# Kernel tuning notes

Measured on AMD Instinct MI355X. Metric: run time of the kernel, lower is better.

Reference implementation:

```python
import jax, jax.numpy as jnp
import numpy as np

T, B, D, H = 256, 64, 1024, 1024


def setup_inputs() -> dict:
    key = jax.random.key(0)
    ks = jax.random.split(key, 12)
    stdv = 1.0 / np.sqrt(H)
    u = lambda k, shape: jax.random.uniform(k, shape, jnp.float32, -stdv, stdv)
    return {
        "input_": jax.random.normal(ks[0], (T, B, D), jnp.float32),
        "length": jax.random.randint(ks[1], (B,), 1, T + 1, jnp.int32),
        "h0": jnp.zeros((B, H), jnp.float32),
        "cj": jax.random.normal(ks[2], (B, H), jnp.float32),
        "he": jax.random.normal(ks[3], (B, H), jnp.float32),
        "w_ih": u(ks[4], (3 * H, D)),
        "w_hh": u(ks[5], (3 * H, H)),
        "w_ch": u(ks[6], (3 * H, H)),
        "w_zh": u(ks[7], (3 * H, H)),
        "b_ih": u(ks[8], (3 * H,)),
        "b_hh": u(ks[9], (3 * H,)),
        "b_ch": u(ks[10], (3 * H,)),
        "b_zh": u(ks[11], (3 * H,)),
    }


def _chunk3(g):
    # mirrors torch .chunk(3, 1) on a (..., 3H) tensor
    return g[..., :H], g[..., H:2 * H], g[..., 2 * H:]


def reference(input_, length, h0, cj, he, w_ih, w_hh, w_ch, w_zh,
              b_ih, b_hh, b_ch, b_zh):
    # context projections are time-invariant: hoist out of the recurrence
    c_r, c_i, c_n = _chunk3(cj @ w_ch.T + b_ch)   # (B,H) each
    z_r, z_i, z_n = _chunk3(he @ w_zh.T + b_zh)   # (B,H) each
    # input projections for all steps at once: (T,B,3H)
    gi_all = jnp.einsum('tbd,gd->tbg', input_, w_ih) + b_ih

    def step(h, xs):
        gi_t, t = xs
        i_r, i_i, i_n = _chunk3(gi_t)
        h_r, h_i, h_n_ = _chunk3(h @ w_hh.T + b_hh)
        resetgate = jax.nn.sigmoid(i_r + h_r + c_r + z_r)
        inputgate = jax.nn.sigmoid(i_i + h_i + c_i + z_i)
        newgate = jnp.tanh(i_n + resetgate * h_n_ + c_n + z_n)
        hy = newgate + inputgate * (h - newgate)
        mask = (t < length).astype(hy.dtype)[:, None]          # (B,1)
        # NOTE: faithful to original torch code, which uses hx[0]
        # (first batch row, broadcast) in the masked branch.
        h_next = hy * mask + h[0] * (1.0 - mask)
        return h_next, h_next

    h_last, output = jax.lax.scan(step, h0, (gi_all, jnp.arange(T)))
    h_n = h_last[None]  # (num_layers=1, B, H)
    return output, h_n
```

## Files before the change

### kernel.cpp

```cpp
#include <hip/hip_runtime.h>
#include <stdint.h>

#define TT 256
#define BB 64
#define DD 1024
#define HH 1024
#define G3 3072

typedef unsigned long long ull;
typedef __attribute__((ext_vector_type(8))) short short8;
typedef __attribute__((ext_vector_type(4))) float f32x4;

__device__ __forceinline__ unsigned short f2bf(float f) {
  union { float f; unsigned int i; } v; v.f = f;
  unsigned int x = v.i;
  return (unsigned short)((x + 0x7fffu + ((x >> 16) & 1u)) >> 16);
}
__device__ __forceinline__ float bf2f(unsigned short u) {
  union { unsigned int i; float f; } v; v.i = ((unsigned int)u) << 16; return v.f;
}
__device__ __forceinline__ f32x4 mfma16(short8 a, short8 b, f32x4 c) {
  return __builtin_amdgcn_mfma_f32_16x16x32_bf16(a, b, c, 0, 0, 0);
}
__device__ __forceinline__ void gload_lds16(const void* g, void* l) {
  __builtin_amdgcn_global_load_lds((const __attribute__((address_space(1))) void*)g,
                                   (__attribute__((address_space(3))) void*)l,
                                   16, 0, 0);
}
__device__ __forceinline__ short8 mall_load16(const unsigned short* p) {
  short8 r;
  asm volatile("global_load_dwordx4 %0, %1, off sc0 sc1" : "=v"(r) : "v"(p));
  return r;
}

__global__ void k_cvt_bf16(const float* __restrict__ in, unsigned short* __restrict__ out, int n4) {
  int i = blockIdx.x * blockDim.x + threadIdx.x;
  int stride = gridDim.x * blockDim.x;
  for (; i < n4; i += stride) {
    float4 v = ((const float4*)in)[i];
    ushort4 o;
    o.x = f2bf(v.x); o.y = f2bf(v.y); o.z = f2bf(v.z); o.w = f2bf(v.w);
    ((ushort4*)out)[i] = o;
  }
}

__global__ __launch_bounds__(256) void k_ctx(
    const unsigned short* __restrict__ cjb, const unsigned short* __restrict__ heb,
    const unsigned short* __restrict__ Wchb, const unsigned short* __restrict__ Wzhb,
    const float* __restrict__ b_ih, const float* __restrict__ b_hh,
    const float* __restrict__ b_ch, const float* __restrict__ b_zh,
    float* __restrict__ E) {
  __shared__ f32x4 red[4][4][64];
  int n0 = blockIdx.x * 16;
  int tid = threadIdx.x;
  int w = tid >> 6, l = tid & 63, lo = l & 15, hi = l >> 4;
  f32x4 acc[4];
#pragma unroll
  for (int r = 0; r < 4; r++) acc[r] = (f32x4){0.f, 0.f, 0.f, 0.f};
#pragma unroll 4
  for (int kk = 0; kk < 16; kk++) {
    int k = w * 512 + kk * 32;
    const unsigned short* Asrc = (k < 1024) ? cjb : heb;
    const unsigned short* Bsrc = (k < 1024) ? Wchb : Wzhb;
    int kw = (k < 1024) ? k : (k - 1024);
    int kof = kw + hi * 8;
    short8 bf = *(const short8*)(Bsrc + (size_t)(n0 + lo) * 1024 + kof);
#pragma unroll
    for (int r = 0; r < 4; r++) {
      short8 af = *(const short8*)(Asrc + (size_t)(r * 16 + lo) * 1024 + kof);
      acc[r] = mfma16(af, bf, acc[r]);
    }
  }
#pragma unroll
  for (int r = 0; r < 4; r++) red[w][r][l] = acc[r];
  __syncthreads();
  f32x4 s = red[0][w][l];
#pragma unroll
  for (int w2 = 1; w2 < 4; w2++) {
    f32x4 p = red[w2][w][l];
    s[0] += p[0]; s[1] += p[1]; s[2] += p[2]; s[3] += p[3];
  }
  int g = n0 + lo;
  float bias = b_ih[g] + b_ch[g] + b_zh[g] + ((g < 2048) ? b_hh[g] : 0.0f);
#pragma unroll
  for (int j = 0; j < 4; j++) {
    int b = w * 16 + hi * 4 + j;
    E[(size_t)b * G3 + g] = s[j] + bias;
  }
}

__global__ __launch_bounds__(256) void k_gemm_gi(
    const unsigned short* __restrict__ Xb,
    const unsigned short* __restrict__ Wb,
    const float* __restrict__ E,
    unsigned short* __restrict__ gi) {
  __shared__ unsigned short As[128 * 32];
  __shared__ unsigned short Bs[128 * 32];
  int bid = blockIdx.x;
  int mt = bid & 127;
  int nt = bid >> 7;
  int m0 = mt * 128, n0 = nt * 128;
  int tid = threadIdx.x;
  int w = tid >> 6, l = tid & 63, lo = l & 15, hi = l >> 4;
  int wr = w >> 1, wc = w & 1;
  f32x4 acc[4][4];
#pragma unroll
  for (int i = 0; i < 4; i++)
#pragma unroll
    for (int j = 0; j < 4; j++) acc[i][j] = (f32x4){0.f, 0.f, 0.f, 0.f};
  int srow = tid >> 2;
  int scol = (tid & 3) * 8;
  for (int kt = 0; kt < 32; kt++) {
    int k0 = kt * 32;
    __syncthreads();
    gload_lds16(Xb + (size_t)(m0 + srow) * 1024 + k0 + scol, As + srow * 32 + scol);
    gload_lds16(Xb + (size_t)(m0 + 64 + srow) * 1024 + k0 + scol, As + (64 + srow) * 32 + scol);
    gload_lds16(Wb + (size_t)(n0 + srow) * 1024 + k0 + scol, Bs + srow * 32 + scol);
    gload_lds16(Wb + (size_t)(n0 + 64 + srow) * 1024 + k0 + scol, Bs + (64 + srow) * 32 + scol);
    asm volatile("s_waitcnt vmcnt(0)" ::: "memory");
    __syncthreads();
    short8 a[4], b[4];
#pragma unroll
    for (int i = 0; i < 4; i++) a[i] = *(const short8*)(As + (wr * 64 + i * 16 + lo) * 32 + hi * 8);
#pragma unroll
    for (int i = 0; i < 4; i++) b[i] = *(const short8*)(Bs + (wc * 64 + i * 16 + lo) * 32 + hi * 8);
#pragma unroll
    for (int i = 0; i < 4; i++)
#pragma unroll
      for (int j = 0; j < 4; j++) acc[i][j] = mfma16(a[i], b[j], acc[i][j]);
  }
#pragma unroll
  for (int i = 0; i < 4; i++)
#pragma unroll
    for (int j = 0; j < 4; j++)
#pragma unroll
      for (int e = 0; e < 4; e++) {
        int r = m0 + wr * 64 + i * 16 + hi * 4 + e;
        int c = n0 + wc * 64 + j * 16 + lo;
        float v = acc[i][j][e] + E[(size_t)(r & 63) * G3 + c];
        gi[(size_t)r * G3 + c] = f2bf(v);
      }
}

__global__ __launch_bounds__(128) void k_rnn(
    const unsigned short* __restrict__ giE,
    const unsigned short* __restrict__ Whhb,
    const float* __restrict__ b_hh,
    const float* __restrict__ h0,
    const int* __restrict__ length,
    unsigned short* __restrict__ hbuf,
    float* __restrict__ out,
    float* __restrict__ hn,
    unsigned int* __restrict__ seq) {
  extern __shared__ char smem[];
  unsigned short* wlds = (unsigned short*)smem;
  float* h0f = (float*)(smem + 98304);

  const int cs = blockIdx.x, j0 = cs * 16;
  const int tid = threadIdx.x;
  const int w = tid >> 6, l = tid & 63, lo = l & 15, hi = l >> 4;
  const int rowbase = w * 32;
  const int col = j0 + lo;

#pragma unroll
  for (int k2 = 0; k2 < 16; ++k2) {
    int kk = w * 16 + k2;
#pragma unroll
    for (int s = 0; s < 3; ++s) {
      int f = kk * 3 + s;
      short8 v = *(const short8*)(Whhb + (size_t)(s * 1024 + j0 + lo) * 1024 + kk * 32 + hi * 8);
      ((short8*)wlds)[f * 64 + l] = v;
    }
  }
  const float bhhn = b_hh[2048 + col];
  float hA[4], hB[4];
  int lenA[4], lenB[4];
#pragma unroll
  for (int j = 0; j < 4; ++j) {
    int rA = rowbase + hi * 4 + j, rB = rA + 16;
    hA[j] = h0[(size_t)rA * 1024 + col]; lenA[j] = length[rA];
    hB[j] = h0[(size_t)rB * 1024 + col]; lenB[j] = length[rB];
  }
  {
    unsigned short* dst = hbuf + (size_t)cs * 1024;
#pragma unroll
    for (int j = 0; j < 4; ++j) {
      unsigned int mA = f2bf(hA[j]), mB = f2bf(hB[j]);
      unsigned int oA = __shfl_xor(mA, 1, 64), oB = __shfl_xor(mB, 1, 64);
      if (!(lo & 1)) {
        int rr = rowbase + hi * 4 + j;
        __hip_atomic_store((unsigned int*)(dst + rr * 16 + lo), mA | (oA << 16),
                           __ATOMIC_RELAXED, __HIP_MEMORY_SCOPE_AGENT);
        __hip_atomic_store((unsigned int*)(dst + (rr + 16) * 16 + lo), mB | (oB << 16),
                           __ATOMIC_RELAXED, __HIP_MEMORY_SCOPE_AGENT);
      }
    }
  }
  if (w == 0 && hi == 0) h0f[lo] = hA[0];
  __syncthreads();
  asm volatile("s_waitcnt vmcnt(0)" ::: "memory");
  if (l == 0)
    __hip_atomic_store(&seq[(cs * 2 + w) * 16], 1u, __ATOMIC_RELAXED, __HIP_MEMORY_SCOPE_AGENT);
  unsigned short gir[24];
#pragma unroll
  for (int r2 = 0; r2 < 2; ++r2)
#pragma unroll
    for (int s = 0; s < 3; ++s)
#pragma unroll
      for (int j = 0; j < 4; ++j)
        gir[(r2 * 3 + s) * 4 + j] =
            giE[(size_t)(rowbase + r2 * 16 + hi * 4 + j) * G3 + s * 1024 + col];

#define ISSUE(c, X)                                                                    \
  _Pragma("unroll") for (int k2 = 0; k2 < 8; ++k2) {                                   \
    int kk = (c) * 8 + k2;                                                             \
    size_t cb = (size_t)(kk * 2 + (hi >> 1));                                          \
    X[k2 * 2 + 0] = mall_load16(base + (cb * 64 + rowbase + lo) * 16 + (hi & 1) * 8);  \
    X[k2 * 2 + 1] = mall_load16(base + (cb * 64 + rowbase + 16 + lo) * 16 + (hi & 1) * 8); \
  }
#define WAITV(N)                                                                       \
  asm volatile("s_waitcnt vmcnt(" #N ")" ::: "memory");                                \
  __builtin_amdgcn_sched_barrier(0)
#define CRUNCH(c, X)                                                                   \
  _Pragma("unroll") for (int k2 = 0; k2 < 8; ++k2) {                                   \
    int kk = (c) * 8 + k2;                                                             \
    const short8* wf = ((const short8*)wlds) + (size_t)(kk * 3) * 64 + l;              \
    short8 b0 = wf[0], b1 = wf[64], b2 = wf[128];                                      \
    a00 = mfma16(X[k2 * 2 + 0], b0, a00);                                              \
    a01 = mfma16(X[k2 * 2 + 0], b1, a01);                                              \
    a02 = mfma16(X[k2 * 2 + 0], b2, a02);                                              \
    a10 = mfma16(X[k2 * 2 + 1], b0, a10);                                              \
    a11 = mfma16(X[k2 * 2 + 1], b1, a11);                                              \
    a12 = mfma16(X[k2 * 2 + 1], b2, a12);                                              \
  }

  for (int t = 0; t < TT; ++t) {
    {
      const unsigned int* sp0 = seq + (size_t)(2 * l) * 16;
      const unsigned int* sp1 = sp0 + 16;
      unsigned int tgt = (unsigned int)(t + 1);
      for (;;) {
        unsigned int v0 = __hip_atomic_load(sp0, __ATOMIC_RELAXED, __HIP_MEMORY_SCOPE_AGENT);
        unsigned int v1 = __hip_atomic_load(sp1, __ATOMIC_RELAXED, __HIP_MEMORY_SCOPE_AGENT);
        if (__all((v0 >= tgt) && (v1 >= tgt))) break;
        __builtin_amdgcn_s_sleep(1);
      }
    }
    const unsigned short* base = hbuf + ((size_t)(t & 1) * 64) * 1024;
    f32x4 a00 = {0.f, 0.f, 0.f, 0.f}, a01 = a00, a02 = a00, a10 = a00, a11 = a00, a12 = a00;
    {
      short8 XA[16], XB[16];
      ISSUE(0, XA);
      ISSUE(1, XB);
      WAITV(16);
      CRUNCH(0, XA);
      ISSUE(2, XA);
      WAITV(16);
      CRUNCH(1, XB);
      ISSUE(3, XB);
      WAITV(16);
      CRUNCH(2, XA);
      WAITV(0);
      CRUNCH(3, XB);
    }
    float h0p = (w == 0) ? __shfl(hA[0], lo, 64) : h0f[(t & 1) * 16 + lo];
    float rA[4], rB[4];
#pragma unroll
    for (int j = 0; j < 4; ++j) {
      float R = a00[j] + bf2f(gir[0 * 4 + j]);
      float I = a01[j] + bf2f(gir[1 * 4 + j]);
      float rg = 1.f / (1.f + __expf(-R));
      float ig = 1.f / (1.f + __expf(-I));
      float nx = bf2f(gir[2 * 4 + j]) + rg * (a02[j] + bhhn);
      nx = fminf(15.f, fmaxf(-15.f, nx));
      float e2 = __expf(2.f * nx);
      float ng = (e2 - 1.f) / (e2 + 1.f);
      float hy = ng + ig * (hA[j] - ng);
      rA[j] = (t < lenA[j]) ? hy : h0p;
    }
#pragma unroll
    for (int j = 0; j < 4; ++j) {
      float R = a10[j] + bf2f(gir[(3 + 0) * 4 + j]);
      float I = a11[j] + bf2f(gir[(3 + 1) * 4 + j]);
      float rg = 1.f / (1.f + __expf(-R));
      float ig = 1.f / (1.f + __expf(-I));
      float nx = bf2f(gir[(3 + 2) * 4 + j]) + rg * (a12[j] + bhhn);
      nx = fminf(15.f, fmaxf(-15.f, nx));
      float e2 = __expf(2.f * nx);
      float ng = (e2 - 1.f) / (e2 + 1.f);
      float hy = ng + ig * (hB[j] - ng);
      rB[j] = (t < lenB[j]) ? hy : h0p;
    }
#pragma unroll
    for (int j = 0; j < 4; ++j) { hA[j] = rA[j]; hB[j] = rB[j]; }
    if (t < TT - 1) {
      unsigned short* dst = hbuf + ((size_t)((t + 1) & 1) * 64 + cs) * 1024;
#pragma unroll
      for (int j = 0; j < 4; ++j) {
        unsigned int mA = f2bf(hA[j]), mB = f2bf(hB[j]);
        unsigned int oA = __shfl_xor(mA, 1, 64), oB = __shfl_xor(mB, 1, 64);
        if (!(lo & 1)) {
          int rr = rowbase + hi * 4 + j;
          __hip_atomic_store((unsigned int*)(dst + rr * 16 + lo), mA | (oA << 16),
                             __ATOMIC_RELAXED, __HIP_MEMORY_SCOPE_AGENT);
          __hip_atomic_store((unsigned int*)(dst + (rr + 16) * 16 + lo), mB | (oB << 16),
                             __ATOMIC_RELAXED, __HIP_MEMORY_SCOPE_AGENT);
        }
      }
      if (w == 0 && hi == 0) h0f[((t + 1) & 1) * 16 + lo] = hA[0];
      asm volatile("s_waitcnt vmcnt(0) lgkmcnt(0)" ::: "memory");
      if (l == 0)
        __hip_atomic_store(&seq[(cs * 2 + w) * 16], (unsigned int)(t + 2),
                           __ATOMIC_RELAXED, __HIP_MEMORY_SCOPE_AGENT);
#pragma unroll
      for (int j = 0; j < 4; ++j) {
        int rr = rowbase + hi * 4 + j;
        out[(size_t)t * (BB * HH) + (size_t)rr * 1024 + col] = rA[j];
        out[(size_t)t * (BB * HH) + (size_t)(rr + 16) * 1024 + col] = rB[j];
      }
      const unsigned short* gb = giE + (size_t)(t + 1) * 64 * G3;
#pragma unroll
      for (int r2 = 0; r2 < 2; ++r2)
#pragma unroll
        for (int s = 0; s < 3; ++s)
#pragma unroll
          for (int j = 0; j < 4; ++j)
            gir[(r2 * 3 + s) * 4 + j] =
                gb[(size_t)(rowbase + r2 * 16 + hi * 4 + j) * G3 + s * 1024 + col];
    } else {
#pragma unroll
      for (int j = 0; j < 4; ++j) {
        int rr = rowbase + hi * 4 + j;
        out[(size_t)t * (BB * HH) + (size_t)rr * 1024 + col] = rA[j];
        out[(size_t)t * (BB * HH) + (size_t)(rr + 16) * 1024 + col] = rB[j];
        hn[(size_t)rr * 1024 + col] = rA[j];
        hn[(size_t)(rr + 16) * 1024 + col] = rB[j];
      }
    }
  }
#undef ISSUE
#undef WAITV
#undef CRUNCH
}

extern "C" void kernel_launch(void* const* d_in, const int* in_sizes, int n_in,
                              void* d_out, int out_size, void* d_ws, size_t ws_size,
                              hipStream_t stream) {
  const float* input_ = (const float*)d_in[0];
  const int* length   = (const int*)d_in[1];
  const float* h0     = (const float*)d_in[2];
  const float* cj     = (const float*)d_in[3];
  const float* he     = (const float*)d_in[4];
  const float* w_ih   = (const float*)d_in[5];
  const float* w_hh   = (const float*)d_in[6];
  const float* w_ch   = (const float*)d_in[7];
  const float* w_zh   = (const float*)d_in[8];
  const float* b_ih   = (const float*)d_in[9];
  const float* b_hh   = (const float*)d_in[10];
  const float* b_ch   = (const float*)d_in[11];
  const float* b_zh   = (const float*)d_in[12];

  char* ws = (char*)d_ws;
  const size_t OFF_SEQ   = 0;
  const size_t OFF_HBUF  = 16384;
  const size_t OFF_XB    = 524288;
  const size_t OFF_WIHB  = OFF_XB + 33554432ull;
  const size_t OFF_WHHB  = OFF_WIHB + 6291456ull;
  const size_t OFF_WCHB  = OFF_WHHB + 6291456ull;
  const size_t OFF_WZHB  = OFF_WCHB + 6291456ull;
  const size_t OFF_CJB   = OFF_WZHB + 6291456ull;
  const size_t OFF_HEB   = OFF_CJB + 131072ull;
  const size_t OFF_E     = OFF_HEB + 131072ull;
  const size_t OFF_GI    = OFF_E + 786432ull;

  unsigned int* seq     = (unsigned int*)(ws + OFF_SEQ);
  unsigned short* hbuf  = (unsigned short*)(ws + OFF_HBUF);
  unsigned short* Xb    = (unsigned short*)(ws + OFF_XB);
  unsigned short* Wihb  = (unsigned short*)(ws + OFF_WIHB);
  unsigned short* Whhb  = (unsigned short*)(ws + OFF_WHHB);
  unsigned short* Wchb  = (unsigned short*)(ws + OFF_WCHB);
  unsigned short* Wzhb  = (unsigned short*)(ws + OFF_WZHB);
  unsigned short* cjb   = (unsigned short*)(ws + OFF_CJB);
  unsigned short* heb   = (unsigned short*)(ws + OFF_HEB);
  float* E              = (float*)(ws + OFF_E);
  unsigned short* gi    = (unsigned short*)(ws + OFF_GI);

  float* out = (float*)d_out;
  float* hn  = out + 16777216;

  hipFuncSetAttribute((const void*)k_rnn, hipFuncAttributeMaxDynamicSharedMemorySize, 98432);

  hipMemsetAsync(seq, 0, 16384, stream);
  k_cvt_bf16<<<2048, 256, 0, stream>>>(input_, Xb, 16777216 / 4);
  k_cvt_bf16<<<1024, 256, 0, stream>>>(w_ih, Wihb, 3145728 / 4);
  k_cvt_bf16<<<1024, 256, 0, stream>>>(w_hh, Whhb, 3145728 / 4);
  k_cvt_bf16<<<1024, 256, 0, stream>>>(w_ch, Wchb, 3145728 / 4);
  k_cvt_bf16<<<1024, 256, 0, stream>>>(w_zh, Wzhb, 3145728 / 4);
  k_cvt_bf16<<<64, 256, 0, stream>>>(cj, cjb, 65536 / 4);
  k_cvt_bf16<<<64, 256, 0, stream>>>(he, heb, 65536 / 4);
  k_ctx<<<192, 256, 0, stream>>>(cjb, heb, Wchb, Wzhb, b_ih, b_hh, b_ch, b_zh, E);
  k_gemm_gi<<<3072, 256, 0, stream>>>(Xb, Wihb, E, gi);
  k_rnn<<<64, 128, 98432, stream>>>(gi, Whhb, b_hh, h0, length, hbuf, out, hn, seq);
}
```

Baseline: 1.408 ms.

## Read recurrent state from fp32 output instead of separate bf16 exchange buffer

Removes the bf16 hbuf handoff buffer. Each block now publishes its fp32 hidden state into the output tensor with atomic stores, and every block reads the previous step's fp32 rows from the output tensor, converting to bf16 in registers with packed conversion instructions. This drops the separate bf16 pack-and-store and the duplicate output write. In exchange, each step reads twice the bytes, the explicit staged load/MFMA pipelining is replaced by a simple unrolled loop, and the loads no longer carry cache-bypass flags, which may risk reading stale data across blocks.

```diff
diff --git a/kernel.cpp b/kernel.cpp
--- a/kernel.cpp
+++ b/kernel.cpp
@@ -27,10 +27,18 @@
                                    (__attribute__((address_space(3))) void*)l,
                                    16, 0, 0);
 }
-__device__ __forceinline__ short8 mall_load16(const unsigned short* p) {
-  short8 r;
-  asm volatile("global_load_dwordx4 %0, %1, off sc0 sc1" : "=v"(r) : "v"(p));
+__device__ __forceinline__ unsigned int cvtpk(float a, float b) {
+  unsigned int r;
+  asm("v_cvt_pk_bf16_f32 %0, %1, %2" : "=v"(r) : "v"(a), "v"(b));
   return r;
+}
+__device__ __forceinline__ short8 pack8(float4 f0, float4 f1) {
+  union { unsigned int u[4]; short8 v; } r;
+  r.u[0] = cvtpk(f0.x, f0.y);
+  r.u[1] = cvtpk(f0.z, f0.w);
+  r.u[2] = cvtpk(f1.x, f1.y);
+  r.u[3] = cvtpk(f1.z, f1.w);
+  return r.v;
 }
 
 __global__ void k_cvt_bf16(const float* __restrict__ in, unsigned short* __restrict__ out, int n4) {
@@ -148,7 +156,6 @@
     const float* __restrict__ b_hh,
     const float* __restrict__ h0,
     const int* __restrict__ length,
-    unsigned short* __restrict__ hbuf,
     float* __restrict__ out,
     float* __restrict__ hn,
     unsigned int* __restrict__ seq) {
@@ -181,24 +188,8 @@
     hA[j] = h0[(size_t)rA * 1024 + col]; lenA[j] = length[rA];
     hB[j] = h0[(size_t)rB * 1024 + col]; lenB[j] = length[rB];
   }
-  {
-    unsigned short* dst = hbuf + (size_t)cs * 1024;
-#pragma unroll
-    for (int j = 0; j < 4; ++j) {
-      unsigned int mA = f2bf(hA[j]), mB = f2bf(hB[j]);
-      unsigned int oA = __shfl_xor(mA, 1, 64), oB = __shfl_xor(mB, 1, 64);
-      if (!(lo & 1)) {
-        int rr = rowbase + hi * 4 + j;
-        __hip_atomic_store((unsigned int*)(dst + rr * 16 + lo), mA | (oA << 16),
-                           __ATOMIC_RELAXED, __HIP_MEMORY_SCOPE_AGENT);
-        __hip_atomic_store((unsigned int*)(dst + (rr + 16) * 16 + lo), mB | (oB << 16),
-                           __ATOMIC_RELAXED, __HIP_MEMORY_SCOPE_AGENT);
-      }
-    }
-  }
   if (w == 0 && hi == 0) h0f[lo] = hA[0];
   __syncthreads();
-  asm volatile("s_waitcnt vmcnt(0)" ::: "memory");
   if (l == 0)
     __hip_atomic_store(&seq[(cs * 2 + w) * 16], 1u, __ATOMIC_RELAXED, __HIP_MEMORY_SCOPE_AGENT);
   unsigned short gir[24];
@@ -210,29 +201,6 @@
       for (int j = 0; j < 4; ++j)
         gir[(r2 * 3 + s) * 4 + j] =
             giE[(size_t)(rowbase + r2 * 16 + hi * 4 + j) * G3 + s * 1024 + col];
-
-#define ISSUE(c, X)                                                                    \
-  _Pragma("unroll") for (int k2 = 0; k2 < 8; ++k2) {                                   \
-    int kk = (c) * 8 + k2;                                                             \
-    size_t cb = (size_t)(kk * 2 + (hi >> 1));                                          \
-    X[k2 * 2 + 0] = mall_load16(base + (cb * 64 + rowbase + lo) * 16 + (hi & 1) * 8);  \
-    X[k2 * 2 + 1] = mall_load16(base + (cb * 64 + rowbase + 16 + lo) * 16 + (hi & 1) * 8); \
-  }
-#define WAITV(N)                                                                       \
-  asm volatile("s_waitcnt vmcnt(" #N ")" ::: "memory");                                \
-  __builtin_amdgcn_sched_barrier(0)
-#define CRUNCH(c, X)                                                                   \
-  _Pragma("unroll") for (int k2 = 0; k2 < 8; ++k2) {                                   \
-    int kk = (c) * 8 + k2;                                                             \
-    const short8* wf = ((const short8*)wlds) + (size_t)(kk * 3) * 64 + l;              \
-    short8 b0 = wf[0], b1 = wf[64], b2 = wf[128];                                      \
-    a00 = mfma16(X[k2 * 2 + 0], b0, a00);                                              \
-    a01 = mfma16(X[k2 * 2 + 0], b1, a01);                                              \
-    a02 = mfma16(X[k2 * 2 + 0], b2, a02);                                              \
-    a10 = mfma16(X[k2 * 2 + 1], b0, a10);                                              \
-    a11 = mfma16(X[k2 * 2 + 1], b1, a11);                                              \
-    a12 = mfma16(X[k2 * 2 + 1], b2, a12);                                              \
-  }
 
   for (int t = 0; t < TT; ++t) {
     {
@@ -246,22 +214,26 @@
         __builtin_amdgcn_s_sleep(1);
       }
     }
-    const unsigned short* base = hbuf + ((size_t)(t & 1) * 64) * 1024;
+    const float* src = (t == 0) ? h0 : (out + (size_t)(t - 1) * (BB * HH));
     f32x4 a00 = {0.f, 0.f, 0.f, 0.f}, a01 = a00, a02 = a00, a10 = a00, a11 = a00, a12 = a00;
-    {
-      short8 XA[16], XB[16];
-      ISSUE(0, XA);
-      ISSUE(1, XB);
-      WAITV(16);
-      CRUNCH(0, XA);
-      ISSUE(2, XA);
-      WAITV(16);
-      CRUNCH(1, XB);
-      ISSUE(3, XB);
-      WAITV(16);
-      CRUNCH(2, XA);
-      WAITV(0);
-      CRUNCH(3, XB);
+#pragma unroll
+    for (int kk = 0; kk < 32; ++kk) {
+      const float* pA = src + (size_t)(rowbase + lo) * 1024 + kk * 32 + hi * 8;
+      const float* pB = pA + 16 * 1024;
+      float4 fA0 = *(const float4*)pA;
+      float4 fA1 = *(const float4*)(pA + 4);
+      float4 fB0 = *(const float4*)pB;
+      float4 fB1 = *(const float4*)(pB + 4);
+      short8 fa = pack8(fA0, fA1);
+      short8 fb = pack8(fB0, fB1);
+      const short8* wf = ((const short8*)wlds) + (size_t)(kk * 3) * 64 + l;
+      short8 b0 = wf[0], b1 = wf[64], b2 = wf[128];
+      a00 = mfma16(fa, b0, a00);
+      a01 = mfma16(fa, b1, a01);
+      a02 = mfma16(fa, b2, a02);
+      a10 = mfma16(fb, b0, a10);
+      a11 = mfma16(fb, b1, a11);
+      a12 = mfma16(fb, b2, a12);
     }
     float h0p = (w == 0) ? __shfl(hA[0], lo, 64) : h0f[(t & 1) * 16 + lo];
     float rA[4], rB[4];
@@ -293,31 +265,23 @@
     }
 #pragma unroll
     for (int j = 0; j < 4; ++j) { hA[j] = rA[j]; hB[j] = rB[j]; }
+    {
+      float* dst = out + (size_t)t * (BB * HH);
+#pragma unroll
+      for (int j = 0; j < 4; ++j) {
+        int rr = rowbase + hi * 4 + j;
+        __hip_atomic_store(dst + (size_t)rr * 1024 + col, rA[j],
+                           __ATOMIC_RELAXED, __HIP_MEMORY_SCOPE_AGENT);
+        __hip_atomic_store(dst + (size_t)(rr + 16) * 1024 + col, rB[j],
+                           __ATOMIC_RELAXED, __HIP_MEMORY_SCOPE_AGENT);
+      }
+    }
+    if (w == 0 && hi == 0) h0f[((t + 1) & 1) * 16 + lo] = rA[0];
     if (t < TT - 1) {
-      unsigned short* dst = hbuf + ((size_t)((t + 1) & 1) * 64 + cs) * 1024;
-#pragma unroll
-      for (int j = 0; j < 4; ++j) {
-        unsigned int mA = f2bf(hA[j]), mB = f2bf(hB[j]);
-        unsigned int oA = __shfl_xor(mA, 1, 64), oB = __shfl_xor(mB, 1, 64);
-        if (!(lo & 1)) {
-          int rr = rowbase + hi * 4 + j;
-          __hip_atomic_store((unsigned int*)(dst + rr * 16 + lo), mA | (oA << 16),
-                             __ATOMIC_RELAXED, __HIP_MEMORY_SCOPE_AGENT);
-          __hip_atomic_store((unsigned int*)(dst + (rr + 16) * 16 + lo), mB | (oB << 16),
-                             __ATOMIC_RELAXED, __HIP_MEMORY_SCOPE_AGENT);
-        }
-      }
-      if (w == 0 && hi == 0) h0f[((t + 1) & 1) * 16 + lo] = hA[0];
       asm volatile("s_waitcnt vmcnt(0) lgkmcnt(0)" ::: "memory");
       if (l == 0)
         __hip_atomic_store(&seq[(cs * 2 + w) * 16], (unsigned int)(t + 2),
                            __ATOMIC_RELAXED, __HIP_MEMORY_SCOPE_AGENT);
-#pragma unroll
-      for (int j = 0; j < 4; ++j) {
-        int rr = rowbase + hi * 4 + j;
-        out[(size_t)t * (BB * HH) + (size_t)rr * 1024 + col] = rA[j];
-        out[(size_t)t * (BB * HH) + (size_t)(rr + 16) * 1024 + col] = rB[j];
-      }
       const unsigned short* gb = giE + (size_t)(t + 1) * 64 * G3;
 #pragma unroll
       for (int r2 = 0; r2 < 2; ++r2)
@@ -331,16 +295,11 @@
 #pragma unroll
       for (int j = 0; j < 4; ++j) {
         int rr = rowbase + hi * 4 + j;
-        out[(size_t)t * (BB * HH) + (size_t)rr * 1024 + col] = rA[j];
-        out[(size_t)t * (BB * HH) + (size_t)(rr + 16) * 1024 + col] = rB[j];
         hn[(size_t)rr * 1024 + col] = rA[j];
         hn[(size_t)(rr + 16) * 1024 + col] = rB[j];
       }
     }
   }
-#undef ISSUE
-#undef WAITV
-#undef CRUNCH
 }
 
 extern "C" void kernel_launch(void* const* d_in, const int* in_sizes, int n_in,
@@ -362,7 +321,6 @@
 
   char* ws = (char*)d_ws;
   const size_t OFF_SEQ   = 0;
-  const size_t OFF_HBUF  = 16384;
   const size_t OFF_XB    = 524288;
   const size_t OFF_WIHB  = OFF_XB + 33554432ull;
   const size_t OFF_WHHB  = OFF_WIHB + 6291456ull;
@@ -374,7 +332,6 @@
   const size_t OFF_GI    = OFF_E + 786432ull;
 
   unsigned int* seq     = (unsigned int*)(ws + OFF_SEQ);
-  unsigned short* hbuf  = (unsigned short*)(ws + OFF_HBUF);
   unsigned short* Xb    = (unsigned short*)(ws + OFF_XB);
   unsigned short* Wihb  = (unsigned short*)(ws + OFF_WIHB);
   unsigned short* Whhb  = (unsigned short*)(ws + OFF_WHHB);
@@ -400,5 +357,5 @@
   k_cvt_bf16<<<64, 256, 0, stream>>>(he, heb, 65536 / 4);
   k_ctx<<<192, 256, 0, stream>>>(cjb, heb, Wchb, Wzhb, b_ih, b_hh, b_ch, b_zh, E);
   k_gemm_gi<<<3072, 256, 0, stream>>>(Xb, Wihb, E, gi);
-  k_rnn<<<64, 128, 98432, stream>>>(gi, Whhb, b_hh, h0, length, hbuf, out, hn, seq);
-}
+  k_rnn<<<64, 128, 98432, stream>>>(gi, Whhb, b_hh, h0, length, out, hn, seq);
+}
```

New measurement: 5.212 ms. +270.2%, slower.

## Fuse input-projection GEMM with recurrence kernel using per-tile ready flags

Applied to the files above, without the earlier changes.

Merges the gi GEMM and the recurrent kernel into one persistent launch. Blocks 0-63 run the recurrence while 192 extra blocks compute GEMM tiles in time order, publish them with cache-bypassing stores, and bump per-row-tile ready counters that the recurrent blocks poll before reading each timestep pair. The aim is to overlap the large input-projection GEMM with the serial recurrence instead of running them back to back. The cost is that the recurrence blocks now use 256-thread blocks with half the threads exiting early, and the GEMM runs on fewer blocks with scalar uncached stores. It also relies on all 256 blocks being co-resident.

```diff
diff --git a/kernel.cpp b/kernel.cpp
--- a/kernel.cpp
+++ b/kernel.cpp
@@ -31,6 +31,10 @@
   short8 r;
   asm volatile("global_load_dwordx4 %0, %1, off sc0 sc1" : "=v"(r) : "v"(p));
   return r;
+}
+__device__ __forceinline__ void mall_store_u16(unsigned short* p, unsigned short v) {
+  unsigned int vv = v;
+  asm volatile("global_store_short %0, %1, off sc0 sc1" :: "v"(p), "v"(vv) : "memory");
 }
 
 __global__ void k_cvt_bf16(const float* __restrict__ in, unsigned short* __restrict__ out, int n4) {
@@ -89,61 +93,11 @@
   }
 }
 
-__global__ __launch_bounds__(256) void k_gemm_gi(
+__global__ __launch_bounds__(256) void k_fused(
     const unsigned short* __restrict__ Xb,
-    const unsigned short* __restrict__ Wb,
+    const unsigned short* __restrict__ Wihb,
     const float* __restrict__ E,
-    unsigned short* __restrict__ gi) {
-  __shared__ unsigned short As[128 * 32];
-  __shared__ unsigned short Bs[128 * 32];
-  int bid = blockIdx.x;
-  int mt = bid & 127;
-  int nt = bid >> 7;
-  int m0 = mt * 128, n0 = nt * 128;
-  int tid = threadIdx.x;
-  int w = tid >> 6, l = tid & 63, lo = l & 15, hi = l >> 4;
-  int wr = w >> 1, wc = w & 1;
-  f32x4 acc[4][4];
-#pragma unroll
-  for (int i = 0; i < 4; i++)
-#pragma unroll
-    for (int j = 0; j < 4; j++) acc[i][j] = (f32x4){0.f, 0.f, 0.f, 0.f};
-  int srow = tid >> 2;
-  int scol = (tid & 3) * 8;
-  for (int kt = 0; kt < 32; kt++) {
-    int k0 = kt * 32;
-    __syncthreads();
-    gload_lds16(Xb + (size_t)(m0 + srow) * 1024 + k0 + scol, As + srow * 32 + scol);
-    gload_lds16(Xb + (size_t)(m0 + 64 + srow) * 1024 + k0 + scol, As + (64 + srow) * 32 + scol);
-    gload_lds16(Wb + (size_t)(n0 + srow) * 1024 + k0 + scol, Bs + srow * 32 + scol);
-    gload_lds16(Wb + (size_t)(n0 + 64 + srow) * 1024 + k0 + scol, Bs + (64 + srow) * 32 + scol);
-    asm volatile("s_waitcnt vmcnt(0)" ::: "memory");
-    __syncthreads();
-    short8 a[4], b[4];
-#pragma unroll
-    for (int i = 0; i < 4; i++) a[i] = *(const short8*)(As + (wr * 64 + i * 16 + lo) * 32 + hi * 8);
-#pragma unroll
-    for (int i = 0; i < 4; i++) b[i] = *(const short8*)(Bs + (wc * 64 + i * 16 + lo) * 32 + hi * 8);
-#pragma unroll
-    for (int i = 0; i < 4; i++)
-#pragma unroll
-      for (int j = 0; j < 4; j++) acc[i][j] = mfma16(a[i], b[j], acc[i][j]);
-  }
-#pragma unroll
-  for (int i = 0; i < 4; i++)
-#pragma unroll
-    for (int j = 0; j < 4; j++)
-#pragma unroll
-      for (int e = 0; e < 4; e++) {
-        int r = m0 + wr * 64 + i * 16 + hi * 4 + e;
-        int c = n0 + wc * 64 + j * 16 + lo;
-        float v = acc[i][j][e] + E[(size_t)(r & 63) * G3 + c];
-        gi[(size_t)r * G3 + c] = f2bf(v);
-      }
-}
-
-__global__ __launch_bounds__(128) void k_rnn(
-    const unsigned short* __restrict__ giE,
+    unsigned short* __restrict__ gi,
     const unsigned short* __restrict__ Whhb,
     const float* __restrict__ b_hh,
     const float* __restrict__ h0,
@@ -151,37 +105,96 @@
     unsigned short* __restrict__ hbuf,
     float* __restrict__ out,
     float* __restrict__ hn,
-    unsigned int* __restrict__ seq) {
+    unsigned int* __restrict__ seq,
+    unsigned int* __restrict__ ready) {
   extern __shared__ char smem[];
+  const int tid = threadIdx.x;
+
+  if (blockIdx.x >= 64) {
+    unsigned short* As = (unsigned short*)smem;
+    unsigned short* Bs = As + 128 * 32;
+    const int b = blockIdx.x - 64;
+    const int w = tid >> 6, l = tid & 63, lo = l & 15, hi = l >> 4;
+    const int wr = w >> 1, wc = w & 1;
+    const int srow = tid >> 2;
+    const int scol = (tid & 3) * 8;
+    for (int i = 0; i < 16; ++i) {
+      int tau = i * 192 + b;
+      int mt = tau / 24, nt = tau - mt * 24;
+      int m0 = mt * 128, n0 = nt * 128;
+      f32x4 acc[4][4];
+#pragma unroll
+      for (int ii = 0; ii < 4; ii++)
+#pragma unroll
+        for (int j = 0; j < 4; j++) acc[ii][j] = (f32x4){0.f, 0.f, 0.f, 0.f};
+      for (int kt = 0; kt < 32; kt++) {
+        int k0 = kt * 32;
+        __syncthreads();
+        gload_lds16(Xb + (size_t)(m0 + srow) * 1024 + k0 + scol, As + srow * 32 + scol);
+        gload_lds16(Xb + (size_t)(m0 + 64 + srow) * 1024 + k0 + scol, As + (64 + srow) * 32 + scol);
+        gload_lds16(Wihb + (size_t)(n0 + srow) * 1024 + k0 + scol, Bs + srow * 32 + scol);
+        gload_lds16(Wihb + (size_t)(n0 + 64 + srow) * 1024 + k0 + scol, Bs + (64 + srow) * 32 + scol);
+        asm volatile("s_waitcnt vmcnt(0)" ::: "memory");
+        __syncthreads();
+        short8 a[4], bb[4];
+#pragma unroll
+        for (int ii = 0; ii < 4; ii++) a[ii] = *(const short8*)(As + (wr * 64 + ii * 16 + lo) * 32 + hi * 8);
+#pragma unroll
+        for (int ii = 0; ii < 4; ii++) bb[ii] = *(const short8*)(Bs + (wc * 64 + ii * 16 + lo) * 32 + hi * 8);
+#pragma unroll
+        for (int ii = 0; ii < 4; ii++)
+#pragma unroll
+          for (int j = 0; j < 4; j++) acc[ii][j] = mfma16(a[ii], bb[j], acc[ii][j]);
+      }
+#pragma unroll
+      for (int ii = 0; ii < 4; ii++)
+#pragma unroll
+        for (int j = 0; j < 4; j++)
+#pragma unroll
+          for (int e = 0; e < 4; e++) {
+            int r = m0 + wr * 64 + ii * 16 + hi * 4 + e;
+            int c = n0 + wc * 64 + j * 16 + lo;
+            float v = acc[ii][j][e] + E[(size_t)(r & 63) * G3 + c];
+            mall_store_u16(gi + (size_t)r * G3 + c, f2bf(v));
+          }
+      asm volatile("s_waitcnt vmcnt(0)" ::: "memory");
+      __syncthreads();
+      if (tid == 0)
+        __hip_atomic_fetch_add(&ready[mt * 16], 1u, __ATOMIC_RELAXED, __HIP_MEMORY_SCOPE_AGENT);
+    }
+    return;
+  }
+
   unsigned short* wlds = (unsigned short*)smem;
   float* h0f = (float*)(smem + 98304);
 
   const int cs = blockIdx.x, j0 = cs * 16;
-  const int tid = threadIdx.x;
   const int w = tid >> 6, l = tid & 63, lo = l & 15, hi = l >> 4;
   const int rowbase = w * 32;
   const int col = j0 + lo;
 
-#pragma unroll
-  for (int k2 = 0; k2 < 16; ++k2) {
-    int kk = w * 16 + k2;
-#pragma unroll
-    for (int s = 0; s < 3; ++s) {
-      int f = kk * 3 + s;
-      short8 v = *(const short8*)(Whhb + (size_t)(s * 1024 + j0 + lo) * 1024 + kk * 32 + hi * 8);
-      ((short8*)wlds)[f * 64 + l] = v;
-    }
-  }
-  const float bhhn = b_hh[2048 + col];
-  float hA[4], hB[4];
-  int lenA[4], lenB[4];
-#pragma unroll
-  for (int j = 0; j < 4; ++j) {
-    int rA = rowbase + hi * 4 + j, rB = rA + 16;
-    hA[j] = h0[(size_t)rA * 1024 + col]; lenA[j] = length[rA];
-    hB[j] = h0[(size_t)rB * 1024 + col]; lenB[j] = length[rB];
-  }
-  {
+  float bhhn = 0.f;
+  float hA[4] = {0,0,0,0}, hB[4] = {0,0,0,0};
+  int lenA[4] = {0,0,0,0}, lenB[4] = {0,0,0,0};
+
+  if (tid < 128) {
+#pragma unroll
+    for (int k2 = 0; k2 < 16; ++k2) {
+      int kk = w * 16 + k2;
+#pragma unroll
+      for (int s = 0; s < 3; ++s) {
+        int f = kk * 3 + s;
+        short8 v = *(const short8*)(Whhb + (size_t)(s * 1024 + j0 + lo) * 1024 + kk * 32 + hi * 8);
+        ((short8*)wlds)[f * 64 + l] = v;
+      }
+    }
+    bhhn = b_hh[2048 + col];
+#pragma unroll
+    for (int j = 0; j < 4; ++j) {
+      int rA = rowbase + hi * 4 + j, rB = rA + 16;
+      hA[j] = h0[(size_t)rA * 1024 + col]; lenA[j] = length[rA];
+      hB[j] = h0[(size_t)rB * 1024 + col]; lenB[j] = length[rB];
+    }
     unsigned short* dst = hbuf + (size_t)cs * 1024;
 #pragma unroll
     for (int j = 0; j < 4; ++j) {
@@ -195,13 +208,28 @@
                            __ATOMIC_RELAXED, __HIP_MEMORY_SCOPE_AGENT);
       }
     }
-  }
-  if (w == 0 && hi == 0) h0f[lo] = hA[0];
+    if (w == 0 && hi == 0) h0f[lo] = hA[0];
+  }
   __syncthreads();
+  if (tid >= 128) return;
   asm volatile("s_waitcnt vmcnt(0)" ::: "memory");
   if (l == 0)
     __hip_atomic_store(&seq[(cs * 2 + w) * 16], 1u, __ATOMIC_RELAXED, __HIP_MEMORY_SCOPE_AGENT);
+
+#define POLL_READY(MT)                                                                  \
+  {                                                                                     \
+    const unsigned int* rp = ready + (size_t)(MT) * 16;                                 \
+    for (;;) {                                                                          \
+      unsigned int v = __hip_atomic_load(rp, __ATOMIC_RELAXED, __HIP_MEMORY_SCOPE_AGENT);\
+      if (v >= 24u) break;                                                              \
+      __builtin_amdgcn_s_sleep(1);                                                      \
+    }                                                                                   \
+    asm volatile("" ::: "memory");                                                      \
+    __builtin_amdgcn_sched_barrier(0);                                                  \
+  }
+
   unsigned short gir[24];
+  POLL_READY(0);
 #pragma unroll
   for (int r2 = 0; r2 < 2; ++r2)
 #pragma unroll
@@ -209,7 +237,7 @@
 #pragma unroll
       for (int j = 0; j < 4; ++j)
         gir[(r2 * 3 + s) * 4 + j] =
-            giE[(size_t)(rowbase + r2 * 16 + hi * 4 + j) * G3 + s * 1024 + col];
+            gi[(size_t)(rowbase + r2 * 16 + hi * 4 + j) * G3 + s * 1024 + col];
 
 #define ISSUE(c, X)                                                                    \
   _Pragma("unroll") for (int k2 = 0; k2 < 8; ++k2) {                                   \
@@ -318,7 +346,8 @@
         out[(size_t)t * (BB * HH) + (size_t)rr * 1024 + col] = rA[j];
         out[(size_t)t * (BB * HH) + (size_t)(rr + 16) * 1024 + col] = rB[j];
       }
-      const unsigned short* gb = giE + (size_t)(t + 1) * 64 * G3;
+      if (((t + 1) & 1) == 0) { POLL_READY((t + 1) >> 1); }
+      const unsigned short* gb = gi + (size_t)(t + 1) * 64 * G3;
 #pragma unroll
       for (int r2 = 0; r2 < 2; ++r2)
 #pragma unroll
@@ -341,6 +370,7 @@
 #undef ISSUE
 #undef WAITV
 #undef CRUNCH
+#undef POLL_READY
 }
 
 extern "C" void kernel_launch(void* const* d_in, const int* in_sizes, int n_in,
@@ -362,7 +392,8 @@
 
   char* ws = (char*)d_ws;
   const size_t OFF_SEQ   = 0;
-  const size_t OFF_HBUF  = 16384;
+  const size_t OFF_READY = 16384;
+  const size_t OFF_HBUF  = 32768;
   const size_t OFF_XB    = 524288;
   const size_t OFF_WIHB  = OFF_XB + 33554432ull;
   const size_t OFF_WHHB  = OFF_WIHB + 6291456ull;
@@ -374,6 +405,7 @@
   const size_t OFF_GI    = OFF_E + 786432ull;
 
   unsigned int* seq     = (unsigned int*)(ws + OFF_SEQ);
+  unsigned int* ready   = (unsigned int*)(ws + OFF_READY);
   unsigned short* hbuf  = (unsigned short*)(ws + OFF_HBUF);
   unsigned short* Xb    = (unsigned short*)(ws + OFF_XB);
   unsigned short* Wihb  = (unsigned short*)(ws + OFF_WIHB);
@@ -388,9 +420,9 @@
   float* out = (float*)d_out;
   float* hn  = out + 16777216;
 
-  hipFuncSetAttribute((const void*)k_rnn, hipFuncAttributeMaxDynamicSharedMemorySize, 98432);
-
-  hipMemsetAsync(seq, 0, 16384, stream);
+  hipFuncSetAttribute((const void*)k_fused, hipFuncAttributeMaxDynamicSharedMemorySize, 98432);
+
+  hipMemsetAsync(ws, 0, 24576, stream);
   k_cvt_bf16<<<2048, 256, 0, stream>>>(input_, Xb, 16777216 / 4);
   k_cvt_bf16<<<1024, 256, 0, stream>>>(w_ih, Wihb, 3145728 / 4);
   k_cvt_bf16<<<1024, 256, 0, stream>>>(w_hh, Whhb, 3145728 / 4);
@@ -399,6 +431,6 @@
   k_cvt_bf16<<<64, 256, 0, stream>>>(cj, cjb, 65536 / 4);
   k_cvt_bf16<<<64, 256, 0, stream>>>(he, heb, 65536 / 4);
   k_ctx<<<192, 256, 0, stream>>>(cjb, heb, Wchb, Wzhb, b_ih, b_hh, b_ch, b_zh, E);
-  k_gemm_gi<<<3072, 256, 0, stream>>>(Xb, Wihb, E, gi);
-  k_rnn<<<64, 128, 98432, stream>>>(gi, Whhb, b_hh, h0, length, hbuf, out, hn, seq);
-}
+  k_fused<<<256, 256, 98432, stream>>>(Xb, Wihb, E, gi, Whhb, b_hh, h0, length,
+                                       hbuf, out, hn, seq, ready);
+}
```

Result: no change. 1.433 ms (+1.8%).
